# Kernel optimization log

Hardware: AMD Instinct MI355X
Metric: run time of the kernel (lower is better)

Reference implementation:

```python
import jax, jax.numpy as jnp
import numpy as np

N, K = 50000, 64          # nodes, anchors per node
E = N * K                 # anchor-set edges
IN_DIM, OUT_DIM = 256, 64


def setup_inputs() -> dict:
    key = jax.random.key(0)
    ks = jax.random.split(key, 12)
    s = 0.02
    return {
        "feature": jax.random.normal(ks[0], (N, IN_DIM), jnp.float32),
        "src": jax.random.randint(ks[1], (E,), 0, N),
        "dst": jax.random.randint(ks[2], (E,), 0, N),
        "sp_dist": jax.random.uniform(ks[3], (E, 1), jnp.float32),
        "anchor_eid": jax.random.randint(ks[4], (N * K,), 0, E),
        "dists_max": jax.random.uniform(ks[5], (N, K), jnp.float32),
        "W_u": jax.random.normal(ks[6], (IN_DIM, OUT_DIM), jnp.float32) * s,
        "b_u": jnp.zeros((OUT_DIM,), jnp.float32),
        "W_v": jax.random.normal(ks[7], (IN_DIM, OUT_DIM), jnp.float32) * s,
        "b_v": jnp.zeros((OUT_DIM,), jnp.float32),
        "W_out": jax.random.normal(ks[8], (OUT_DIM, 1), jnp.float32) * s,
        "b_out": jnp.zeros((1,), jnp.float32),
    }


def reference(feature, src, dst, sp_dist, anchor_eid, dists_max,
              W_u, b_u, W_v, b_v, W_out, b_out):
    # node-level linear projections: [N, OUT_DIM]
    u_feat = feature @ W_u + b_u
    v_feat = feature @ W_v + b_v
    # edge message: v_feat[dst] + u_feat[src] * sp_dist  -> [E, OUT_DIM]
    message = v_feat[dst] + u_feat[src] * sp_dist
    # gather anchor edges and reshape to [N, K, OUT_DIM]
    msgs = jax.nn.relu(
        message[anchor_eid].reshape(dists_max.shape[0], dists_max.shape[1], -1)
    )
    out_position = (msgs @ W_out + b_out)[..., 0]  # [N, K]
    out_structure = jnp.mean(msgs, axis=1)         # [N, OUT_DIM]
    return out_position, out_structure
```

## Files before the change

kernel.cpp:

```cpp
#include <hip/hip_runtime.h>
#include <hip/hip_fp16.h>
#include <hip/hip_bf16.h>


#define IN_DIM 256
#define OUT_DIM 64
#define KANCH 64

typedef float vfloat4 __attribute__((ext_vector_type(4)));
typedef float vfloat2 __attribute__((ext_vector_type(2)));

#define PAa 68
#define PBb 132
#define TILEF (16 * PAa + 16 * PBb)
__global__ __launch_bounds__(256) void pgnn_front_kernel(
    const float* __restrict__ feature,
    const float* __restrict__ Wu, const float* __restrict__ bu,
    const float* __restrict__ Wv, const float* __restrict__ bv,
    unsigned char* __restrict__ uq8,
    __half* __restrict__ vh16,
    const int* __restrict__ src, const int* __restrict__ dst,
    const float* __restrict__ sp,
    unsigned long long* __restrict__ meta,
    int N, int E, int projBlocks)
{
    __shared__ float smem[2 * TILEF];
    const int tid = threadIdx.x;

    if ((int)blockIdx.x >= projBlocks) {
        int i = (blockIdx.x - projBlocks) * 256 + tid;
        if (i >= E) return;
        unsigned long long pk =
              (unsigned long long)(unsigned)__builtin_nontemporal_load(&src[i])
            | ((unsigned long long)(unsigned)__builtin_nontemporal_load(&dst[i]) << 17)
            | ((unsigned long long)__half_as_ushort(
                   __float2half_rn(__builtin_nontemporal_load(&sp[i]))) << 34);
        __builtin_nontemporal_store(pk, &meta[i]);
        return;
    }

    const int row0 = blockIdx.x * 64;
    const int tr = tid >> 4;
    const int tc = tid & 15;
    const int mA = tid >> 2, c4A = tid & 3;
    const int grA = row0 + mA;

    float accU[4][4], accV[4][4];
    #pragma unroll
    for (int i = 0; i < 4; ++i)
        #pragma unroll
        for (int j = 0; j < 4; ++j) { accU[i][j] = 0.f; accV[i][j] = 0.f; }

    float4 ra, rb0, rb1;
    auto load_tile = [&](int k0) {
        ra = make_float4(0.f, 0.f, 0.f, 0.f);
        if (grA < N)
            ra = *reinterpret_cast<const float4*>(
                    &feature[(size_t)grA * IN_DIM + k0 + c4A * 4]);
        {
            int f = tid, kk = f >> 5, c4 = f & 31;
            rb0 = (c4 < 16)
                ? *reinterpret_cast<const float4*>(&Wu[(k0 + kk) * OUT_DIM + c4 * 4])
                : *reinterpret_cast<const float4*>(&Wv[(k0 + kk) * OUT_DIM + (c4 - 16) * 4]);
        }
        {
            int f = tid + 256, kk = f >> 5, c4 = f & 31;
            rb1 = (c4 < 16)
                ? *reinterpret_cast<const float4*>(&Wu[(k0 + kk) * OUT_DIM + c4 * 4])
                : *reinterpret_cast<const float4*>(&Wv[(k0 + kk) * OUT_DIM + (c4 - 16) * 4]);
        }
    };
    auto store_tile = [&](float* buf) {
        buf[(c4A * 4 + 0) * PAa + mA] = ra.x;
        buf[(c4A * 4 + 1) * PAa + mA] = ra.y;
        buf[(c4A * 4 + 2) * PAa + mA] = ra.z;
        buf[(c4A * 4 + 3) * PAa + mA] = ra.w;
        float* sB = buf + 16 * PAa;
        {
            int f = tid, kk = f >> 5, c4 = f & 31;
            *reinterpret_cast<float4*>(&sB[kk * PBb + c4 * 4]) = rb0;
        }
        {
            int f = tid + 256, kk = f >> 5, c4 = f & 31;
            *reinterpret_cast<float4*>(&sB[kk * PBb + c4 * 4]) = rb1;
        }
    };

    load_tile(0);
    store_tile(smem);
    __syncthreads();

    for (int s = 0; s < 16; ++s) {
        const int cur = s & 1;
        if (s < 15) load_tile((s + 1) * 16);
        const float* buf = smem + cur * TILEF;
        const float* sB  = buf + 16 * PAa;
        #pragma unroll
        for (int k = 0; k < 16; ++k) {
            float4 a  = *reinterpret_cast<const float4*>(&buf[k * PAa + tr * 4]);
            float4 b0 = *reinterpret_cast<const float4*>(&sB[k * PBb + tc * 4]);
            float4 b1 = *reinterpret_cast<const float4*>(&sB[k * PBb + 64 + tc * 4]);
            float av[4]  = {a.x, a.y, a.z, a.w};
            float bu4[4] = {b0.x, b0.y, b0.z, b0.w};
            float bv4[4] = {b1.x, b1.y, b1.z, b1.w};
            #pragma unroll
            for (int i = 0; i < 4; ++i)
                #pragma unroll
                for (int j = 0; j < 4; ++j) {
                    accU[i][j] = fmaf(av[i], bu4[j], accU[i][j]);
                    accV[i][j] = fmaf(av[i], bv4[j], accV[i][j]);
                }
        }
        if (s < 15) store_tile(smem + (cur ^ 1) * TILEF);
        __syncthreads();
    }

    const int qs   = tc >> 3;
    const int offq = (tc & 7) * 4;
    float bU[4], bV[4];
    #pragma unroll
    for (int j = 0; j < 4; ++j) { bU[j] = bu[tc * 4 + j]; bV[j] = bv[tc * 4 + j]; }
    #pragma unroll
    for (int i = 0; i < 4; ++i) {
        int gr = row0 + tr * 4 + i;
        if (gr >= N) continue;
        unsigned char* urow = uq8 + ((size_t)qs * N + gr) * 32;
        int pu = 0;
        pu = __builtin_amdgcn_cvt_pk_fp8_f32(accU[i][0] + bU[0],
                                             accU[i][1] + bU[1], pu, false);
        pu = __builtin_amdgcn_cvt_pk_fp8_f32(accU[i][2] + bU[2],
                                             accU[i][3] + bU[3], pu, true);
        *reinterpret_cast<unsigned int*>(urow + offq) = (unsigned)pu;

        __half* vrow = vh16 + ((size_t)qs * N + gr) * 32;
        __half2 hv0 = __floats2half2_rn(accV[i][0] + bV[0], accV[i][1] + bV[1]);
        __half2 hv1 = __floats2half2_rn(accV[i][2] + bV[2], accV[i][3] + bV[3]);
        *reinterpret_cast<__half2*>(vrow + offq)     = hv0;
        *reinterpret_cast<__half2*>(vrow + offq + 2) = hv1;
    }
}

template<int META, bool FIRST>
__global__ __launch_bounds__(256) void pgnn_pass_kernel(
    const unsigned char* __restrict__ uq8,
    const __half* __restrict__ vh16,
    const int*    __restrict__ src,
    const int*    __restrict__ dst,
    const float*  __restrict__ sp_dist,
    const int*    __restrict__ aeid,
    unsigned long long* __restrict__ packed,
    const unsigned long long* __restrict__ meta,
    const float*  __restrict__ W_out,
    const float*  __restrict__ b_out,
    float* __restrict__ out_pos,
    float* __restrict__ out_struct,
    int N, int q)
{
    const int lane = threadIdx.x & 63;
    const int wv   = threadIdx.x >> 6;
    const int n    = blockIdx.x * 4 + wv;
    if (n >= N) return;

    __shared__ float posb[4][64];
    float* pb = posb[wv];

    const int j = lane & 3, g = lane >> 2;

    int ms, md; float msp;
    if constexpr (META == 2) {
        const int e = __builtin_nontemporal_load(&aeid[(size_t)n * KANCH + lane]);
        ms = src[e]; md = dst[e]; msp = sp_dist[e];
    } else {
        unsigned long long pk;
        if constexpr (META == 1) {
            const int e = __builtin_nontemporal_load(&aeid[(size_t)n * KANCH + lane]);
            pk = meta[e];
            __builtin_nontemporal_store(pk, &packed[(size_t)n * KANCH + lane]);
        } else {
            pk = __builtin_nontemporal_load(&packed[(size_t)n * KANCH + lane]);
        }
        unsigned lo = (unsigned)pk, hi = (unsigned)(pk >> 32);
        ms = (int)(lo & 0x1FFFFu);
        md = (int)(((lo >> 17) | (hi << 15)) & 0x1FFFFu);
        msp = __half2float(__ushort_as_half((unsigned short)((hi >> 2) & 0xFFFFu)));
    }

    float w[8];
    {
        const float* Wq = &W_out[q * 32 + j * 8];
        float4 w0 = *reinterpret_cast<const float4*>(Wq);
        float4 w1 = *reinterpret_cast<const float4*>(Wq + 4);
        w[0] = w0.x; w[1] = w0.y; w[2] = w0.z; w[3] = w0.w;
        w[4] = w1.x; w[5] = w1.y; w[6] = w1.z; w[7] = w1.w;
    }

    const unsigned char* Uq = uq8  + (size_t)q * N * 32;
    const __half*        Vq = vh16 + (size_t)q * N * 32;

    float sacc[8];
    #pragma unroll
    for (int jj = 0; jj < 8; ++jj) sacc[jj] = 0.f;

    #pragma unroll
    for (int i = 0; i < 4; ++i) {
        const int k = i * 16 + g;
        const int   ss = __shfl(ms, k);
        const int   dd = __shfl(md, k);
        const float sp = __shfl(msp, k);

        uint2 uu = *reinterpret_cast<const uint2*>(Uq + (size_t)ss * 32 + j * 8);
        uint4 vv = *reinterpret_cast<const uint4*>(
                       reinterpret_cast<const unsigned char*>(Vq) +
                       (size_t)dd * 64 + j * 16);

        float uf[8], vf[8];
        {
            vfloat2 a0 = __builtin_amdgcn_cvt_pk_f32_fp8((int)uu.x, false);
            vfloat2 a1 = __builtin_amdgcn_cvt_pk_f32_fp8((int)uu.x, true);
            vfloat2 a2 = __builtin_amdgcn_cvt_pk_f32_fp8((int)uu.y, false);
            vfloat2 a3 = __builtin_amdgcn_cvt_pk_f32_fp8((int)uu.y, true);
            uf[0] = a0.x; uf[1] = a0.y; uf[2] = a1.x; uf[3] = a1.y;
            uf[4] = a2.x; uf[5] = a2.y; uf[6] = a3.x; uf[7] = a3.y;
        }
        {
            const unsigned* vp = &vv.x;
            #pragma unroll
            for (int t = 0; t < 4; ++t) {
                __half2 h2 = *reinterpret_cast<const __half2*>(&vp[t]);
                float2 f2 = __half22float2(h2);
                vf[2 * t] = f2.x; vf[2 * t + 1] = f2.y;
            }
        }

        float m[8];
        #pragma unroll
        for (int jj = 0; jj < 8; ++jj) {
            m[jj] = fmaxf(fmaf(uf[jj], sp, vf[jj]), 0.f);
            sacc[jj] += m[jj];
        }

        float p = 0.f;
        #pragma unroll
        for (int jj = 0; jj < 8; ++jj) p = fmaf(m[jj], w[jj], p);
        p += __shfl_xor(p, 1);
        p += __shfl_xor(p, 2);
        if (j == 0) pb[k] = p;
    }
    asm volatile("s_waitcnt lgkmcnt(0)" ::: "memory");

    if constexpr (FIRST) {
        out_pos[(size_t)n * KANCH + lane] = pb[lane] + b_out[0];
    } else {
        atomicAdd(&out_pos[(size_t)n * KANCH + lane], pb[lane]);
    }

    #pragma unroll
    for (int off = 4; off <= 32; off <<= 1)
        #pragma unroll
        for (int jj = 0; jj < 8; ++jj)
            sacc[jj] += __shfl_xor(sacc[jj], off);

    if (lane < 4) {
        const float r = 1.f / (float)KANCH;
        float* op = &out_struct[(size_t)n * OUT_DIM + q * 32 + lane * 8];
        vfloat4 s0 = { sacc[0] * r, sacc[1] * r, sacc[2] * r, sacc[3] * r };
        vfloat4 s1 = { sacc[4] * r, sacc[5] * r, sacc[6] * r, sacc[7] * r };
        __builtin_nontemporal_store(s0, reinterpret_cast<vfloat4*>(op));
        __builtin_nontemporal_store(s1, reinterpret_cast<vfloat4*>(op + 4));
    }
}

extern "C" void kernel_launch(void* const* d_in, const int* in_sizes, int n_in,
                              void* d_out, int out_size, void* d_ws, size_t ws_size,
                              hipStream_t stream) {
    const float* feature    = (const float*)d_in[0];
    const int*   src        = (const int*)  d_in[1];
    const int*   dst        = (const int*)  d_in[2];
    const float* sp_dist    = (const float*)d_in[3];
    const int*   anchor_eid = (const int*)  d_in[4];
    const float* W_u   = (const float*)d_in[6];
    const float* b_u   = (const float*)d_in[7];
    const float* W_v   = (const float*)d_in[8];
    const float* b_v   = (const float*)d_in[9];
    const float* W_out = (const float*)d_in[10];
    const float* b_out = (const float*)d_in[11];

    const int N = in_sizes[0] / IN_DIM;
    const int E = in_sizes[1];
    const int M = N * KANCH;

    unsigned char* uq8 = (unsigned char*)d_ws;
    size_t uq8_bytes  = (size_t)N * 64;
    size_t vh_off     = (uq8_bytes + 255) & ~(size_t)255;
    __half* vh16      = (__half*)((char*)d_ws + vh_off);
    size_t vh_bytes   = (size_t)N * 64 * sizeof(__half);
    size_t packed_off = (vh_off + vh_bytes + 255) & ~(size_t)255;
    size_t meta_off   = (packed_off + (size_t)M * 8 + 255) & ~(size_t)255;
    unsigned long long* packed = (unsigned long long*)((char*)d_ws + packed_off);
    unsigned long long* meta   = (unsigned long long*)((char*)d_ws + meta_off);
    const bool fields_fit = (N < (1 << 17));
    const bool use_packed = fields_fit && (ws_size >= meta_off + (size_t)E * 8);

    float* out_pos    = (float*)d_out;
    float* out_struct = (float*)d_out + (size_t)N * KANCH;

    const int projBlocks = (N + 63) / 64;
    const int nblk = (N + 3) / 4;

    if (use_packed) {
        const int mergeBlocks = (E + 255) / 256;
        pgnn_front_kernel<<<dim3(projBlocks + mergeBlocks), 256, 0, stream>>>(
            feature, W_u, b_u, W_v, b_v, uq8, vh16, src, dst, sp_dist, meta,
            N, E, projBlocks);
        pgnn_pass_kernel<1, true><<<dim3(nblk), 256, 0, stream>>>(
            uq8, vh16, src, dst, sp_dist, anchor_eid, packed, meta, W_out,
            b_out, out_pos, out_struct, N, 0);
        pgnn_pass_kernel<0, false><<<dim3(nblk), 256, 0, stream>>>(
            uq8, vh16, src, dst, sp_dist, anchor_eid, packed, meta, W_out,
            b_out, out_pos, out_struct, N, 1);
    } else {
        pgnn_front_kernel<<<dim3(projBlocks), 256, 0, stream>>>(
            feature, W_u, b_u, W_v, b_v, uq8, vh16, src, dst, sp_dist, meta,
            N, 0 , projBlocks);
        pgnn_pass_kernel<2, true><<<dim3(nblk), 256, 0, stream>>>(
            uq8, vh16, src, dst, sp_dist, anchor_eid, packed, meta, W_out,
            b_out, out_pos, out_struct, N, 0);
        pgnn_pass_kernel<2, false><<<dim3(nblk), 256, 0, stream>>>(
            uq8, vh16, src, dst, sp_dist, anchor_eid, packed, meta, W_out,
            b_out, out_pos, out_struct, N, 1);
    }
}
```

Before: 222.0 us.

## Move anchor-meta gather into projection kernel as interleaved pack blocks

Builds the packed src/dst/sp metadata in its own small kernel first. The per-anchor gather of that metadata into a node-ordered buffer moves out of the first pass kernel and into the projection kernel, where every fourth block does the pack. Pack blocks use a grid-stride loop with 8 independent gathers in flight. The aim is to overlap the latency-bound random gather with the compute-bound GEMM and to leave both pass kernels doing plain streaming reads. The cost is an extra kernel launch and GEMM blocks that now share CUs with gather traffic.

```diff
diff --git a/kernel.cpp b/kernel.cpp
--- a/kernel.cpp
+++ b/kernel.cpp
@@ -9,6 +9,20 @@
 
 typedef float vfloat4 __attribute__((ext_vector_type(4)));
 typedef float vfloat2 __attribute__((ext_vector_type(2)));
+
+__global__ __launch_bounds__(256) void pgnn_merge_kernel(
+    const int* __restrict__ src, const int* __restrict__ dst,
+    const float* __restrict__ sp, unsigned long long* __restrict__ meta, int E)
+{
+    int i = blockIdx.x * 256 + threadIdx.x;
+    if (i >= E) return;
+    unsigned long long pk =
+          (unsigned long long)(unsigned)__builtin_nontemporal_load(&src[i])
+        | ((unsigned long long)(unsigned)__builtin_nontemporal_load(&dst[i]) << 17)
+        | ((unsigned long long)__half_as_ushort(
+               __float2half_rn(__builtin_nontemporal_load(&sp[i]))) << 34);
+    __builtin_nontemporal_store(pk, &meta[i]);
+}
 
 #define PAa 68
 #define PBb 132
@@ -19,27 +33,43 @@
     const float* __restrict__ Wv, const float* __restrict__ bv,
     unsigned char* __restrict__ uq8,
     __half* __restrict__ vh16,
-    const int* __restrict__ src, const int* __restrict__ dst,
-    const float* __restrict__ sp,
-    unsigned long long* __restrict__ meta,
-    int N, int E, int projBlocks)
+    const int* __restrict__ aeid,
+    const unsigned long long* __restrict__ meta,
+    unsigned long long* __restrict__ packed,
+    int N, int M, int projBlocks, int packBlocks)
 {
     __shared__ float smem[2 * TILEF];
     const int tid = threadIdx.x;
-
-    if ((int)blockIdx.x >= projBlocks) {
-        int i = (blockIdx.x - projBlocks) * 256 + tid;
-        if (i >= E) return;
-        unsigned long long pk =
-              (unsigned long long)(unsigned)__builtin_nontemporal_load(&src[i])
-            | ((unsigned long long)(unsigned)__builtin_nontemporal_load(&dst[i]) << 17)
-            | ((unsigned long long)__half_as_ushort(
-                   __float2half_rn(__builtin_nontemporal_load(&sp[i]))) << 34);
-        __builtin_nontemporal_store(pk, &meta[i]);
+    const int bidx = (int)blockIdx.x;
+
+    const bool isPack = packBlocks > 0 && (bidx & 3) == 3;
+    if (isPack) {
+        const int pack_id = bidx >> 2;
+        const int stride = packBlocks * 256;
+        int i = pack_id * 256 + tid;
+        while (i + 7 * stride < M) {
+            int e[8];
+            #pragma unroll
+            for (int b = 0; b < 8; ++b)
+                e[b] = __builtin_nontemporal_load(&aeid[i + b * stride]);
+            unsigned long long m[8];
+            #pragma unroll
+            for (int b = 0; b < 8; ++b) m[b] = meta[e[b]];
+            #pragma unroll
+            for (int b = 0; b < 8; ++b)
+                __builtin_nontemporal_store(m[b], &packed[i + b * stride]);
+            i += 8 * stride;
+        }
+        for (; i < M; i += stride) {
+            int e = __builtin_nontemporal_load(&aeid[i]);
+            __builtin_nontemporal_store(meta[e], &packed[i]);
+        }
         return;
     }
 
-    const int row0 = blockIdx.x * 64;
+    const int proj_id = packBlocks > 0 ? bidx - ((bidx + 1) >> 2) : bidx;
+    if (proj_id >= projBlocks) return;
+    const int row0 = proj_id * 64;
     const int tr = tid >> 4;
     const int tc = tid & 15;
     const int mA = tid >> 2, c4A = tid & 3;
@@ -148,8 +178,7 @@
     const int*    __restrict__ dst,
     const float*  __restrict__ sp_dist,
     const int*    __restrict__ aeid,
-    unsigned long long* __restrict__ packed,
-    const unsigned long long* __restrict__ meta,
+    const unsigned long long* __restrict__ packed,
     const float*  __restrict__ W_out,
     const float*  __restrict__ b_out,
     float* __restrict__ out_pos,
@@ -171,14 +200,8 @@
         const int e = __builtin_nontemporal_load(&aeid[(size_t)n * KANCH + lane]);
         ms = src[e]; md = dst[e]; msp = sp_dist[e];
     } else {
-        unsigned long long pk;
-        if constexpr (META == 1) {
-            const int e = __builtin_nontemporal_load(&aeid[(size_t)n * KANCH + lane]);
-            pk = meta[e];
-            __builtin_nontemporal_store(pk, &packed[(size_t)n * KANCH + lane]);
-        } else {
-            pk = __builtin_nontemporal_load(&packed[(size_t)n * KANCH + lane]);
-        }
+        unsigned long long pk =
+            __builtin_nontemporal_load(&packed[(size_t)n * KANCH + lane]);
         unsigned lo = (unsigned)pk, hi = (unsigned)(pk >> 32);
         ms = (int)(lo & 0x1FFFFu);
         md = (int)(((lo >> 17) | (hi << 15)) & 0x1FFFFu);
@@ -308,25 +331,28 @@
     const int nblk = (N + 3) / 4;
 
     if (use_packed) {
-        const int mergeBlocks = (E + 255) / 256;
-        pgnn_front_kernel<<<dim3(projBlocks + mergeBlocks), 256, 0, stream>>>(
-            feature, W_u, b_u, W_v, b_v, uq8, vh16, src, dst, sp_dist, meta,
-            N, E, projBlocks);
-        pgnn_pass_kernel<1, true><<<dim3(nblk), 256, 0, stream>>>(
-            uq8, vh16, src, dst, sp_dist, anchor_eid, packed, meta, W_out,
+        pgnn_merge_kernel<<<dim3((E + 255) / 256), 256, 0, stream>>>(
+            src, dst, sp_dist, meta, E);
+        const int G = (4 * projBlocks + 2) / 3;
+        const int packBlocks = G / 4;
+        pgnn_front_kernel<<<dim3(G), 256, 0, stream>>>(
+            feature, W_u, b_u, W_v, b_v, uq8, vh16, anchor_eid, meta, packed,
+            N, M, projBlocks, packBlocks);
+        pgnn_pass_kernel<0, true><<<dim3(nblk), 256, 0, stream>>>(
+            uq8, vh16, src, dst, sp_dist, anchor_eid, packed, W_out,
             b_out, out_pos, out_struct, N, 0);
         pgnn_pass_kernel<0, false><<<dim3(nblk), 256, 0, stream>>>(
-            uq8, vh16, src, dst, sp_dist, anchor_eid, packed, meta, W_out,
+            uq8, vh16, src, dst, sp_dist, anchor_eid, packed, W_out,
             b_out, out_pos, out_struct, N, 1);
     } else {
         pgnn_front_kernel<<<dim3(projBlocks), 256, 0, stream>>>(
-            feature, W_u, b_u, W_v, b_v, uq8, vh16, src, dst, sp_dist, meta,
-            N, 0 , projBlocks);
+            feature, W_u, b_u, W_v, b_v, uq8, vh16, anchor_eid, meta, packed,
+            N, M, projBlocks, 0 );
         pgnn_pass_kernel<2, true><<<dim3(nblk), 256, 0, stream>>>(
-            uq8, vh16, src, dst, sp_dist, anchor_eid, packed, meta, W_out,
+            uq8, vh16, src, dst, sp_dist, anchor_eid, packed, W_out,
             b_out, out_pos, out_struct, N, 0);
         pgnn_pass_kernel<2, false><<<dim3(nblk), 256, 0, stream>>>(
-            uq8, vh16, src, dst, sp_dist, anchor_eid, packed, meta, W_out,
+            uq8, vh16, src, dst, sp_dist, anchor_eid, packed, W_out,
             b_out, out_pos, out_struct, N, 1);
     }
 }
```

Result: slower. 269.3 us (+21.3%).
